# Kernel tuning notes

Measured on AMD Instinct MI355X. Metric: run time of the kernel, lower is better.

## Reference

```python
import jax, jax.numpy as jnp
import numpy as np

N_NODES = 50000
N_EDGES = 800000
IN_DIM = 128
HID_DIM = 128
N_GRAPHS = 512


def setup_inputs() -> dict:
    key = jax.random.key(0)
    ks = jax.random.split(key, 8)
    x = jax.random.normal(ks[0], (N_NODES, IN_DIM), dtype=jnp.float32)
    edge_index = jax.random.randint(ks[1], (2, N_EDGES), 0, N_NODES, dtype=jnp.int64)
    batch = jnp.sort(jax.random.randint(ks[2], (N_NODES,), 0, N_GRAPHS, dtype=jnp.int64))
    x_source = jax.random.randint(ks[3], (N_NODES,), 0, 2, dtype=jnp.int64)
    s1 = 1.0 / np.sqrt(IN_DIM)
    s2 = 1.0 / np.sqrt(HID_DIM)
    W1 = jax.random.normal(ks[4], (IN_DIM, HID_DIM), dtype=jnp.float32) * s1
    b1 = jnp.zeros((HID_DIM,), dtype=jnp.float32)
    W2 = jax.random.normal(ks[5], (HID_DIM, HID_DIM), dtype=jnp.float32) * s2
    b2 = jnp.zeros((HID_DIM,), dtype=jnp.float32)
    Wh = jax.random.normal(ks[6], (HID_DIM + IN_DIM, 2), dtype=jnp.float32) * (1.0 / np.sqrt(HID_DIM + IN_DIM))
    bh = jnp.zeros((2,), dtype=jnp.float32)
    return {"x": x, "edge_index": edge_index, "batch": batch, "x_source": x_source,
            "W1": W1, "b1": b1, "W2": W2, "b2": b2, "Wh": Wh, "bh": bh}


def _gcn_conv(x, W, b, src, dst, deg_inv_sqrt):
    # PyG GCNConv: h = x W; out[i] = sum_{j->i} norm_ij h[j] + norm_ii h[i] + b
    # with self-loops and symmetric normalization norm_ij = d_i^{-1/2} d_j^{-1/2}
    h = x @ W                                        # [N, out]
    norm_e = deg_inv_sqrt[src] * deg_inv_sqrt[dst]    # [E]
    msg = h[src] * norm_e[:, None]                    # gather + scale
    agg = jax.ops.segment_sum(msg, dst, num_segments=x.shape[0])
    agg = agg + h * (deg_inv_sqrt ** 2)[:, None]      # self-loop term
    return agg + b


def _mean_pool(x, seg, num_segments):
    sums = jax.ops.segment_sum(x, seg, num_segments=num_segments)
    cnt = jax.ops.segment_sum(jnp.ones((x.shape[0],), x.dtype), seg, num_segments=num_segments)
    return sums / jnp.maximum(cnt, 1.0)[:, None]


def reference(x, edge_index, batch, x_source, W1, b1, W2, b2, Wh, bh):
    src, dst = edge_index[0], edge_index[1]
    # degree with self-loops (edge weights = 1)
    deg = jax.ops.segment_sum(jnp.ones((src.shape[0],), x.dtype), dst,
                              num_segments=x.shape[0]) + 1.0
    deg_inv_sqrt = jax.lax.rsqrt(deg)

    h = jax.nn.relu(_gcn_conv(x, W1, b1, src, dst, deg_inv_sqrt))
    # dropout is identity in eval mode
    h = jax.nn.relu(_gcn_conv(h, W2, b2, src, dst, deg_inv_sqrt))

    gnn_emb = _mean_pool(h, batch, N_GRAPHS)          # [G, hid]

    # CodeBERT pooling: masked mean of raw node features where x_source == 1
    mask = (x_source == 1).astype(x.dtype)            # [N]
    summed = jax.ops.segment_sum(x * mask[:, None], batch, num_segments=N_GRAPHS)
    counts = jnp.maximum(jax.ops.segment_sum(mask, batch, num_segments=N_GRAPHS), 1.0)
    codebert_emb = summed / counts[:, None]           # [G, in]

    emb = jnp.concatenate([gnn_emb, codebert_emb], axis=1)  # [G, hid+in]
    return emb @ Wh + bh                              # [G, 2]
```

## Files before the change

### kernel.cpp

```cpp
#include <hip/hip_runtime.h>
#include <hip/hip_fp16.h>

#define NNODES 50000
#define NEDGES 800000
#define DIM    128
#define NGRAPH 512
#define NSLAB  3125
#define EPB    1024
#define NBLK_E 782
#define NBUCK  196
#define HSTRIDE NBLK_E
#define NHIST  (NBUCK * HSTRIDE)
#define NSB1   ((NHIST + 255) / 256)

typedef _Float16 f16x8 __attribute__((ext_vector_type(8)));
typedef float    f32x4 __attribute__((ext_vector_type(4)));
union U4H8 { uint4 u; f16x8 h; };

__global__ void prep_w(const float* __restrict__ W1, const float* __restrict__ W2,
                       __half* __restrict__ Wt1, __half* __restrict__ Wt2) {
    int i = blockIdx.x * 256 + threadIdx.x;
    if (i >= 4096) return;
    const float* W = (i < 2048) ? W1 : W2;
    __half* Wt = (i < 2048) ? Wt1 : Wt2;
    int j = i & 2047;
    int c  = j >> 4;
    int k0 = (j & 15) * 8;
    __half tmp[8];
    #pragma unroll
    for (int u = 0; u < 8; ++u) tmp[u] = (__half)W[(size_t)(k0 + u) * DIM + c];
    *(uint4*)(Wt + (size_t)c * DIM + k0) = *(uint4*)tmp;
}

__global__ void __launch_bounds__(256) bucket_hist(const int* __restrict__ dst,
                                                   int* __restrict__ hist) {
    __shared__ int cnt[NBUCK];
    int t = threadIdx.x;
    if (t < NBUCK) cnt[t] = 0;
    __syncthreads();
    int e0 = blockIdx.x * EPB + t * 4;
    if (e0 + 3 < NEDGES) {
        int4 d = *(const int4*)(dst + e0);
        atomicAdd(&cnt[d.x >> 8], 1);
        atomicAdd(&cnt[d.y >> 8], 1);
        atomicAdd(&cnt[d.z >> 8], 1);
        atomicAdd(&cnt[d.w >> 8], 1);
    }
    __syncthreads();
    if (t < NBUCK) hist[t * HSTRIDE + blockIdx.x] = cnt[t];
}

__global__ void sb1(const int* __restrict__ in, int* __restrict__ out,
                    int* __restrict__ partials) {
    __shared__ int s[256];
    int t = threadIdx.x;
    int gid = blockIdx.x * 256 + t;
    int v = (gid < NHIST) ? in[gid] : 0;
    s[t] = v;
    __syncthreads();
    #pragma unroll
    for (int o = 1; o < 256; o <<= 1) {
        int u = (t >= o) ? s[t - o] : 0;
        __syncthreads();
        s[t] += u;
        __syncthreads();
    }
    if (gid < NHIST) out[gid] = s[t] - v;
    if (t == 255) partials[blockIdx.x] = s[255];
}

__global__ void sb2(int* __restrict__ partials) {
    __shared__ int s[1024];
    int t = threadIdx.x;
    int v = (t < NSB1) ? partials[t] : 0;
    s[t] = v;
    __syncthreads();
    #pragma unroll
    for (int o = 1; o < 1024; o <<= 1) {
        int u = (t >= o) ? s[t - o] : 0;
        __syncthreads();
        s[t] += u;
        __syncthreads();
    }
    if (t < NSB1) partials[t] = s[t] - v;
}

__global__ void sb3(int* __restrict__ hist, const int* __restrict__ partials) {
    int gid = blockIdx.x * 256 + threadIdx.x;
    if (gid < NHIST) hist[gid] += partials[blockIdx.x];
}

__global__ void __launch_bounds__(256) bucket_scatter(const int* __restrict__ src,
                                                      const int* __restrict__ dst,
                                                      const int* __restrict__ hist,
                                                      int2* __restrict__ ebuf) {
    __shared__ int cnt[NBUCK];
    __shared__ int base[NBUCK];
    int t = threadIdx.x;
    if (t < NBUCK) { cnt[t] = 0; base[t] = hist[t * HSTRIDE + blockIdx.x]; }
    __syncthreads();
    int e0 = blockIdx.x * EPB + t * 4;
    if (e0 + 3 < NEDGES) {
        int4 s = *(const int4*)(src + e0);
        int4 d = *(const int4*)(dst + e0);
        int b, r;
        b = d.x >> 8; r = atomicAdd(&cnt[b], 1); ebuf[base[b] + r] = make_int2(s.x, d.x);
        b = d.y >> 8; r = atomicAdd(&cnt[b], 1); ebuf[base[b] + r] = make_int2(s.y, d.y);
        b = d.z >> 8; r = atomicAdd(&cnt[b], 1); ebuf[base[b] + r] = make_int2(s.z, d.z);
        b = d.w >> 8; r = atomicAdd(&cnt[b], 1); ebuf[base[b] + r] = make_int2(s.w, d.w);
    }
}

__global__ void __launch_bounds__(256) node_sort(const int2* __restrict__ ebuf,
                                                 const int* __restrict__ hist,
                                                 int* __restrict__ rowstart,
                                                 float* __restrict__ dis,
                                                 int* __restrict__ csr_src) {
    __shared__ int cnt[256], cnt2[256], off[256], s[256];
    int b = blockIdx.x;
    int t = threadIdx.x;
    int start = hist[b * HSTRIDE];
    int end = (b + 1 < NBUCK) ? hist[(b + 1) * HSTRIDE] : NEDGES;
    cnt[t] = 0; cnt2[t] = 0;
    __syncthreads();
    for (int i = start + t; i < end; i += 256)
        atomicAdd(&cnt[ebuf[i].y & 255], 1);
    __syncthreads();
    s[t] = cnt[t];
    __syncthreads();
    #pragma unroll
    for (int o = 1; o < 256; o <<= 1) {
        int u = (t >= o) ? s[t - o] : 0;
        __syncthreads();
        s[t] += u;
        __syncthreads();
    }
    off[t] = s[t] - cnt[t];
    int node = b * 256 + t;
    if (node < NNODES) {
        rowstart[node] = start + off[t];
        dis[node] = rsqrtf((float)cnt[t] + 1.0f);
    }
    if (b == NBUCK - 1 && t == 0) rowstart[NNODES] = NEDGES;
    __syncthreads();
    for (int i = start + t; i < end; i += 256) {
        int2 e = ebuf[i];
        int j = e.y & 255;
        int r = atomicAdd(&cnt2[j], 1);
        csr_src[start + off[j] + r] = e.x;
    }
}

template<typename XT>
__global__ void __launch_bounds__(256) gemm_mfma(const XT* __restrict__ X,
                                                 const __half* __restrict__ Wt,
                                                 const float* __restrict__ dis,
                                                 __half* __restrict__ Y) {
    __shared__ __align__(16) unsigned char Wl[128 * 256];

    const int t = threadIdx.x;
    {
        int col = t >> 1;
        int kb0 = (t & 1) * 128;
        const unsigned char* g = (const unsigned char*)Wt + col * 256 + kb0;
        #pragma unroll
        for (int i = 0; i < 8; ++i) {
            uint4 v = *(const uint4*)(g + i * 16);
            int kb = kb0 + i * 16;
            *(uint4*)(Wl + col * 256 + (kb ^ ((col & 7) << 4))) = v;
        }
    }
    __syncthreads();

    int wave = t >> 6;
    int slab = blockIdx.x * 4 + wave;
    if (slab >= NSLAB) return;
    int l  = t & 63;
    int lr = l & 15;
    int lg = l >> 4;

    int arow = slab * 16 + lr;

    f16x8 afr[4];
    if constexpr (sizeof(XT) == 4) {
        const float* xr = (const float*)X + (size_t)arow * DIM;
        #pragma unroll
        for (int c = 0; c < 4; ++c) {
            int k0 = c * 32 + lg * 8;
            float4 u0 = *(const float4*)(xr + k0);
            float4 u1 = *(const float4*)(xr + k0 + 4);
            f16x8 a;
            a[0] = (_Float16)u0.x; a[1] = (_Float16)u0.y;
            a[2] = (_Float16)u0.z; a[3] = (_Float16)u0.w;
            a[4] = (_Float16)u1.x; a[5] = (_Float16)u1.y;
            a[6] = (_Float16)u1.z; a[7] = (_Float16)u1.w;
            afr[c] = a;
        }
    } else {
        const __half* xr = (const __half*)X + (size_t)arow * DIM;
        #pragma unroll
        for (int c = 0; c < 4; ++c) {
            U4H8 u; u.u = *(const uint4*)(xr + c * 32 + lg * 8);
            afr[c] = u.h;
        }
    }

    f32x4 acc[8];
    #pragma unroll
    for (int jt = 0; jt < 8; ++jt) acc[jt] = (f32x4){0.f, 0.f, 0.f, 0.f};

    #pragma unroll
    for (int c = 0; c < 4; ++c) {
        #pragma unroll
        for (int jt = 0; jt < 8; ++jt) {
            int col = jt * 16 + lr;
            int kb  = c * 64 + lg * 16;
            U4H8 bb;
            bb.u = *(const uint4*)(Wl + col * 256 + (kb ^ ((col & 7) << 4)));
            acc[jt] = __builtin_amdgcn_mfma_f32_16x16x32_f16(afr[c], bb.h, acc[jt], 0, 0, 0);
        }
    }

    float4 dv = *(const float4*)(dis + slab * 16 + lg * 4);
    float dsc[4] = {dv.x, dv.y, dv.z, dv.w};
    #pragma unroll
    for (int j = 0; j < 4; ++j) {
        int row = slab * 16 + lg * 4 + j;
        __half* yr = Y + (size_t)row * DIM + lr;
        #pragma unroll
        for (int jt = 0; jt < 8; ++jt)
            yr[jt * 16] = (__half)(acc[jt][j] * dsc[j]);
    }
}

__device__ __forceinline__ void acc_add(float4& a, uint2 u) {
    float2 f0 = __half22float2(*(__half2*)&u.x);
    float2 f1 = __half22float2(*(__half2*)&u.y);
    a.x += f0.x; a.y += f0.y; a.z += f1.x; a.w += f1.y;
}

__global__ void __launch_bounds__(256) gcn_gather(const __half* __restrict__ hwh,
                                                  const int* __restrict__ rowstart,
                                                  const int* __restrict__ csr_src,
                                                  const float* __restrict__ dis,
                                                  const float* __restrict__ b,
                                                  __half* __restrict__ outh) {
    int t = blockIdx.x * 256 + threadIdx.x;
    int d = t >> 5, q = t & 31;
    if (d >= NNODES) return;
    const uint2* hw8 = (const uint2*)hwh;

    float4 a0 = make_float4(0.f, 0.f, 0.f, 0.f);
    float4 a1 = a0, a2 = a0, a3 = a0, a4 = a0, a5 = a0, a6 = a0, a7 = a0;

    acc_add(a0, hw8[(size_t)d * 32 + q]);

    int beg = rowstart[d], end = rowstart[d + 1];
    int i = beg;
    for (; i + 8 <= end; i += 8) {
        int s0 = csr_src[i + 0], s1 = csr_src[i + 1];
        int s2 = csr_src[i + 2], s3 = csr_src[i + 3];
        int s4 = csr_src[i + 4], s5 = csr_src[i + 5];
        int s6 = csr_src[i + 6], s7 = csr_src[i + 7];
        uint2 v0 = hw8[(size_t)s0 * 32 + q];
        uint2 v1 = hw8[(size_t)s1 * 32 + q];
        uint2 v2 = hw8[(size_t)s2 * 32 + q];
        uint2 v3 = hw8[(size_t)s3 * 32 + q];
        uint2 v4 = hw8[(size_t)s4 * 32 + q];
        uint2 v5 = hw8[(size_t)s5 * 32 + q];
        uint2 v6 = hw8[(size_t)s6 * 32 + q];
        uint2 v7 = hw8[(size_t)s7 * 32 + q];
        acc_add(a0, v0); acc_add(a1, v1); acc_add(a2, v2); acc_add(a3, v3);
        acc_add(a4, v4); acc_add(a5, v5); acc_add(a6, v6); acc_add(a7, v7);
    }
    for (; i + 2 <= end; i += 2) {
        uint2 v0 = hw8[(size_t)csr_src[i + 0] * 32 + q];
        uint2 v1 = hw8[(size_t)csr_src[i + 1] * 32 + q];
        acc_add(a0, v0); acc_add(a1, v1);
    }
    if (i < end) acc_add(a0, hw8[(size_t)csr_src[i] * 32 + q]);

    a0.x += a1.x + a2.x + a3.x + a4.x + a5.x + a6.x + a7.x;
    a0.y += a1.y + a2.y + a3.y + a4.y + a5.y + a6.y + a7.y;
    a0.z += a1.z + a2.z + a3.z + a4.z + a5.z + a6.z + a7.z;
    a0.w += a1.w + a2.w + a3.w + a4.w + a5.w + a6.w + a7.w;

    float dd = dis[d];
    float4 bb = ((const float4*)b)[q];
    __half ot[4];
    ot[0] = (__half)fmaxf(fmaf(a0.x, dd, bb.x), 0.f);
    ot[1] = (__half)fmaxf(fmaf(a0.y, dd, bb.y), 0.f);
    ot[2] = (__half)fmaxf(fmaf(a0.z, dd, bb.z), 0.f);
    ot[3] = (__half)fmaxf(fmaf(a0.w, dd, bb.w), 0.f);
    ((uint2*)outh)[(size_t)d * 32 + q] = *(uint2*)ot;
}

__device__ __forceinline__ int lower_bound_i(const int* __restrict__ a, int n, int v) {
    int lo = 0, hi = n;
    while (lo < hi) {
        int mid = (lo + hi) >> 1;
        if (a[mid] < v) lo = mid + 1; else hi = mid;
    }
    return lo;
}

__global__ void __launch_bounds__(256) pool_head(const __half* __restrict__ h,
                                                 const float* __restrict__ x,
                                                 const int* __restrict__ batch,
                                                 const int* __restrict__ xsrc,
                                                 const float* __restrict__ Wh,
                                                 const float* __restrict__ bh,
                                                 float* __restrict__ out) {
    __shared__ float sAG[DIM];
    __shared__ float sAC[DIM];
    __shared__ int   sSC;
    int g   = blockIdx.x;
    int t   = threadIdx.x;
    int sub = t >> 5;
    int q   = t & 31;

    if (t < DIM) { sAG[t] = 0.f; sAC[t] = 0.f; }
    if (t == 0) sSC = 0;
    __syncthreads();

    int lo = lower_bound_i(batch, NNODES, g);
    int hi = lower_bound_i(batch, NNODES, g + 1);

    float4 ag = make_float4(0.f, 0.f, 0.f, 0.f);
    float4 ac = make_float4(0.f, 0.f, 0.f, 0.f);
    int sc = 0;
    const uint2* h8 = (const uint2*)h;
    const float4* x4 = (const float4*)x;
    for (int r = lo + sub; r < hi; r += 8) {
        acc_add(ag, h8[(size_t)r * 32 + q]);
        if (xsrc[r] == 1) {
            float4 xv = x4[(size_t)r * 32 + q];
            ac.x += xv.x; ac.y += xv.y; ac.z += xv.z; ac.w += xv.w;
            sc++;
        }
    }
    float* agp = sAG + q * 4;
    atomicAdd(agp + 0, ag.x); atomicAdd(agp + 1, ag.y);
    atomicAdd(agp + 2, ag.z); atomicAdd(agp + 3, ag.w);
    float* acp = sAC + q * 4;
    atomicAdd(acp + 0, ac.x); atomicAdd(acp + 1, ac.y);
    atomicAdd(acp + 2, ac.z); atomicAdd(acp + 3, ac.w);
    if (q == 0 && sc) atomicAdd(&sSC, sc);
    __syncthreads();

    if (t < 32) {
        float invg = 1.0f / fmaxf((float)(hi - lo), 1.0f);
        float invc = 1.0f / fmaxf((float)sSC, 1.0f);
        const float2* Wh2 = (const float2*)Wh;
        float a0 = 0.f, a1 = 0.f;
        #pragma unroll
        for (int j = 0; j < 4; ++j) {
            float e1 = sAG[t * 4 + j] * invg;
            float2 w1 = Wh2[t * 4 + j];
            a0 = fmaf(e1, w1.x, a0);
            a1 = fmaf(e1, w1.y, a1);
            float e2 = sAC[t * 4 + j] * invc;
            float2 w2 = Wh2[DIM + t * 4 + j];
            a0 = fmaf(e2, w2.x, a0);
            a1 = fmaf(e2, w2.y, a1);
        }
        #pragma unroll
        for (int off = 16; off; off >>= 1) {
            a0 += __shfl_down(a0, off, 32);
            a1 += __shfl_down(a1, off, 32);
        }
        if (t == 0) {
            out[g * 2 + 0] = a0 + bh[0];
            out[g * 2 + 1] = a1 + bh[1];
        }
    }
}

extern "C" void kernel_launch(void* const* d_in, const int* in_sizes, int n_in,
                              void* d_out, int out_size, void* d_ws, size_t ws_size,
                              hipStream_t stream) {
    const float* x     = (const float*)d_in[0];
    const int*   ei    = (const int*)d_in[1];
    const int*   batch = (const int*)d_in[2];
    const int*   xsrc  = (const int*)d_in[3];
    const float* W1 = (const float*)d_in[4];
    const float* b1 = (const float*)d_in[5];
    const float* W2 = (const float*)d_in[6];
    const float* b2 = (const float*)d_in[7];
    const float* Wh = (const float*)d_in[8];
    const float* bh = (const float*)d_in[9];
    float* out = (float*)d_out;

    const int* src = ei;
    const int* dst = ei + NEDGES;

    float* ws = (float*)d_ws;
    size_t off = 0;
    float*  dis      = ws + off;            off += 50048;
    int*    rowstart = (int*)(ws + off);    off += 50048;
    int*    hist     = (int*)(ws + off);    off += ((NHIST + 255) & ~255);
    int*    partials = (int*)(ws + off);    off += 1024;
    int2*   ebuf     = (int2*)(ws + off);   off += 2 * 800000;
    int*    csr_src  = (int*)(ws + off);    off += 800000;
    __half* Wt1      = (__half*)(ws + off); off += 8192;
    __half* Wt2      = (__half*)(ws + off); off += 8192;
    __half* hwh      = (__half*)(ws + off); off += (size_t)NNODES * DIM / 2;
    __half* hbuf     = (__half*)(ws + off); off += (size_t)NNODES * DIM / 2;

    prep_w<<<16, 256, 0, stream>>>(W1, W2, Wt1, Wt2);
    bucket_hist<<<NBLK_E, 256, 0, stream>>>(dst, hist);
    sb1<<<NSB1, 256, 0, stream>>>(hist, hist, partials);
    sb2<<<1, 1024, 0, stream>>>(partials);
    sb3<<<NSB1, 256, 0, stream>>>(hist, partials);
    bucket_scatter<<<NBLK_E, 256, 0, stream>>>(src, dst, hist, ebuf);
    node_sort<<<NBUCK, 256, 0, stream>>>(ebuf, hist, rowstart, dis, csr_src);

    const int ngemm = (NSLAB + 3) / 4;

    gemm_mfma<float><<<ngemm, 256, 0, stream>>>(x, Wt1, dis, hwh);
    gcn_gather<<<(NNODES * 32) / 256, 256, 0, stream>>>(hwh, rowstart, csr_src, dis, b1, hbuf);

    gemm_mfma<__half><<<ngemm, 256, 0, stream>>>(hbuf, Wt2, dis, hwh);
    gcn_gather<<<(NNODES * 32) / 256, 256, 0, stream>>>(hwh, rowstart, csr_src, dis, b2, hbuf);

    pool_head<<<NGRAPH, 256, 0, stream>>>(hbuf, x, batch, xsrc, Wh, bh, out);
}
```

Measured before the change: 151.1 us.

## Pack edge buffer to 32 bits, restructure bucket scan, fuse weight prep

Edges in the bucket buffer are now packed into one 32-bit word (16-bit source plus the low 8 bits of the destination) instead of an int2, which halves the traffic of the scatter and node-sort passes. The three-kernel global scan becomes a per-bucket scan plus a small scan of bucket totals. Weight transposition is folded into extra blocks of the histogram kernel, and each block now handles 2048 edges. Together these cut launches and preprocessing traffic, but the packing only works while node ids fit in 16 bits.

Measured after the change: 157.1 us. 1.04x slower.

```diff
diff --git a/kernel.cpp b/kernel.cpp
--- a/kernel.cpp
+++ b/kernel.cpp
@@ -6,56 +6,77 @@
 #define DIM    128
 #define NGRAPH 512
 #define NSLAB  3125
-#define EPB    1024
-#define NBLK_E 782
+#define EPB    2048
+#define NBLK_E 391
 #define NBUCK  196
 #define HSTRIDE NBLK_E
-#define NHIST  (NBUCK * HSTRIDE)
-#define NSB1   ((NHIST + 255) / 256)
 
 typedef _Float16 f16x8 __attribute__((ext_vector_type(8)));
 typedef float    f32x4 __attribute__((ext_vector_type(4)));
 union U4H8 { uint4 u; f16x8 h; };
 
-__global__ void prep_w(const float* __restrict__ W1, const float* __restrict__ W2,
-                       __half* __restrict__ Wt1, __half* __restrict__ Wt2) {
-    int i = blockIdx.x * 256 + threadIdx.x;
-    if (i >= 4096) return;
-    const float* W = (i < 2048) ? W1 : W2;
-    __half* Wt = (i < 2048) ? Wt1 : Wt2;
-    int j = i & 2047;
-    int c  = j >> 4;
-    int k0 = (j & 15) * 8;
-    __half tmp[8];
-    #pragma unroll
-    for (int u = 0; u < 8; ++u) tmp[u] = (__half)W[(size_t)(k0 + u) * DIM + c];
-    *(uint4*)(Wt + (size_t)c * DIM + k0) = *(uint4*)tmp;
-}
-
 __global__ void __launch_bounds__(256) bucket_hist(const int* __restrict__ dst,
-                                                   int* __restrict__ hist) {
+                                                   int* __restrict__ hist,
+                                                   const float* __restrict__ W1,
+                                                   const float* __restrict__ W2,
+                                                   __half* __restrict__ Wt1,
+                                                   __half* __restrict__ Wt2) {
+    int t = threadIdx.x;
+    if (blockIdx.x >= NBLK_E) {
+        int i = (blockIdx.x - NBLK_E) * 256 + t;
+        const float* W = (i < 2048) ? W1 : W2;
+        __half* Wt = (i < 2048) ? Wt1 : Wt2;
+        int j = i & 2047;
+        int c  = j >> 4;
+        int k0 = (j & 15) * 8;
+        __half tmp[8];
+        #pragma unroll
+        for (int u = 0; u < 8; ++u) tmp[u] = (__half)W[(size_t)(k0 + u) * DIM + c];
+        *(uint4*)(Wt + (size_t)c * DIM + k0) = *(uint4*)tmp;
+        return;
+    }
     __shared__ int cnt[NBUCK];
+    if (t < NBUCK) cnt[t] = 0;
+    __syncthreads();
+    int e0 = blockIdx.x * EPB + t * 8;
+    if (e0 + 7 < NEDGES) {
+        int4 d0 = *(const int4*)(dst + e0);
+        int4 d1 = *(const int4*)(dst + e0 + 4);
+        atomicAdd(&cnt[d0.x >> 8], 1);
+        atomicAdd(&cnt[d0.y >> 8], 1);
+        atomicAdd(&cnt[d0.z >> 8], 1);
+        atomicAdd(&cnt[d0.w >> 8], 1);
+        atomicAdd(&cnt[d1.x >> 8], 1);
+        atomicAdd(&cnt[d1.y >> 8], 1);
+        atomicAdd(&cnt[d1.z >> 8], 1);
+        atomicAdd(&cnt[d1.w >> 8], 1);
+    }
+    __syncthreads();
+    if (t < NBUCK) hist[t * HSTRIDE + blockIdx.x] = cnt[t];
+}
+
+__global__ void __launch_bounds__(512) scan1(int* __restrict__ hist, int* __restrict__ btot) {
+    __shared__ int s[512];
+    int b = blockIdx.x;
     int t = threadIdx.x;
-    if (t < NBUCK) cnt[t] = 0;
-    __syncthreads();
-    int e0 = blockIdx.x * EPB + t * 4;
-    if (e0 + 3 < NEDGES) {
-        int4 d = *(const int4*)(dst + e0);
-        atomicAdd(&cnt[d.x >> 8], 1);
-        atomicAdd(&cnt[d.y >> 8], 1);
-        atomicAdd(&cnt[d.z >> 8], 1);
-        atomicAdd(&cnt[d.w >> 8], 1);
-    }
-    __syncthreads();
-    if (t < NBUCK) hist[t * HSTRIDE + blockIdx.x] = cnt[t];
-}
-
-__global__ void sb1(const int* __restrict__ in, int* __restrict__ out,
-                    int* __restrict__ partials) {
+    int v = (t < HSTRIDE) ? hist[b * HSTRIDE + t] : 0;
+    s[t] = v;
+    __syncthreads();
+    #pragma unroll
+    for (int o = 1; o < 512; o <<= 1) {
+        int u = (t >= o) ? s[t - o] : 0;
+        __syncthreads();
+        s[t] += u;
+        __syncthreads();
+    }
+    if (t < HSTRIDE) hist[b * HSTRIDE + t] = s[t] - v;
+    if (t == 511) btot[b] = s[511];
+}
+
+__global__ void __launch_bounds__(256) scan2(const int* __restrict__ btot, int* __restrict__ base) {
     __shared__ int s[256];
     int t = threadIdx.x;
-    int gid = blockIdx.x * 256 + t;
-    int v = (gid < NHIST) ? in[gid] : 0;
+    int v = (t < NBUCK) ? btot[t] : 0;
     s[t] = v;
     __syncthreads();
     #pragma unroll
@@ -65,66 +86,52 @@
         s[t] += u;
         __syncthreads();
     }
-    if (gid < NHIST) out[gid] = s[t] - v;
-    if (t == 255) partials[blockIdx.x] = s[255];
-}
-
-__global__ void sb2(int* __restrict__ partials) {
-    __shared__ int s[1024];
-    int t = threadIdx.x;
-    int v = (t < NSB1) ? partials[t] : 0;
-    s[t] = v;
-    __syncthreads();
-    #pragma unroll
-    for (int o = 1; o < 1024; o <<= 1) {
-        int u = (t >= o) ? s[t - o] : 0;
-        __syncthreads();
-        s[t] += u;
-        __syncthreads();
-    }
-    if (t < NSB1) partials[t] = s[t] - v;
-}
-
-__global__ void sb3(int* __restrict__ hist, const int* __restrict__ partials) {
-    int gid = blockIdx.x * 256 + threadIdx.x;
-    if (gid < NHIST) hist[gid] += partials[blockIdx.x];
+    if (t < NBUCK) base[t] = s[t] - v;
+    if (t == 255) base[NBUCK] = s[255];
 }
 
 __global__ void __launch_bounds__(256) bucket_scatter(const int* __restrict__ src,
                                                       const int* __restrict__ dst,
                                                       const int* __restrict__ hist,
-                                                      int2* __restrict__ ebuf) {
+                                                      const int* __restrict__ base,
+                                                      unsigned* __restrict__ ebuf) {
     __shared__ int cnt[NBUCK];
-    __shared__ int base[NBUCK];
+    __shared__ int sbase[NBUCK];
     int t = threadIdx.x;
-    if (t < NBUCK) { cnt[t] = 0; base[t] = hist[t * HSTRIDE + blockIdx.x]; }
-    __syncthreads();
-    int e0 = blockIdx.x * EPB + t * 4;
-    if (e0 + 3 < NEDGES) {
-        int4 s = *(const int4*)(src + e0);
-        int4 d = *(const int4*)(dst + e0);
+    if (t < NBUCK) { cnt[t] = 0; sbase[t] = base[t] + hist[t * HSTRIDE + blockIdx.x]; }
+    __syncthreads();
+    int e0 = blockIdx.x * EPB + t * 8;
+    if (e0 + 7 < NEDGES) {
+        int4 s0 = *(const int4*)(src + e0);
+        int4 s1 = *(const int4*)(src + e0 + 4);
+        int4 d0 = *(const int4*)(dst + e0);
+        int4 d1 = *(const int4*)(dst + e0 + 4);
         int b, r;
-        b = d.x >> 8; r = atomicAdd(&cnt[b], 1); ebuf[base[b] + r] = make_int2(s.x, d.x);
-        b = d.y >> 8; r = atomicAdd(&cnt[b], 1); ebuf[base[b] + r] = make_int2(s.y, d.y);
-        b = d.z >> 8; r = atomicAdd(&cnt[b], 1); ebuf[base[b] + r] = make_int2(s.z, d.z);
-        b = d.w >> 8; r = atomicAdd(&cnt[b], 1); ebuf[base[b] + r] = make_int2(s.w, d.w);
-    }
-}
-
-__global__ void __launch_bounds__(256) node_sort(const int2* __restrict__ ebuf,
-                                                 const int* __restrict__ hist,
+        b = d0.x >> 8; r = atomicAdd(&cnt[b], 1); ebuf[sbase[b] + r] = (unsigned)s0.x | ((unsigned)(d0.x & 255) << 16);
+        b = d0.y >> 8; r = atomicAdd(&cnt[b], 1); ebuf[sbase[b] + r] = (unsigned)s0.y | ((unsigned)(d0.y & 255) << 16);
+        b = d0.z >> 8; r = atomicAdd(&cnt[b], 1); ebuf[sbase[b] + r] = (unsigned)s0.z | ((unsigned)(d0.z & 255) << 16);
+        b = d0.w >> 8; r = atomicAdd(&cnt[b], 1); ebuf[sbase[b] + r] = (unsigned)s0.w | ((unsigned)(d0.w & 255) << 16);
+        b = d1.x >> 8; r = atomicAdd(&cnt[b], 1); ebuf[sbase[b] + r] = (unsigned)s1.x | ((unsigned)(d1.x & 255) << 16);
+        b = d1.y >> 8; r = atomicAdd(&cnt[b], 1); ebuf[sbase[b] + r] = (unsigned)s1.y | ((unsigned)(d1.y & 255) << 16);
+        b = d1.z >> 8; r = atomicAdd(&cnt[b], 1); ebuf[sbase[b] + r] = (unsigned)s1.z | ((unsigned)(d1.z & 255) << 16);
+        b = d1.w >> 8; r = atomicAdd(&cnt[b], 1); ebuf[sbase[b] + r] = (unsigned)s1.w | ((unsigned)(d1.w & 255) << 16);
+    }
+}
+
+__global__ void __launch_bounds__(256) node_sort(const unsigned* __restrict__ ebuf,
+                                                 const int* __restrict__ base,
                                                  int* __restrict__ rowstart,
                                                  float* __restrict__ dis,
                                                  int* __restrict__ csr_src) {
     __shared__ int cnt[256], cnt2[256], off[256], s[256];
     int b = blockIdx.x;
     int t = threadIdx.x;
-    int start = hist[b * HSTRIDE];
-    int end = (b + 1 < NBUCK) ? hist[(b + 1) * HSTRIDE] : NEDGES;
+    int start = base[b];
+    int end   = base[b + 1];
     cnt[t] = 0; cnt2[t] = 0;
     __syncthreads();
     for (int i = start + t; i < end; i += 256)
-        atomicAdd(&cnt[ebuf[i].y & 255], 1);
+        atomicAdd(&cnt[(ebuf[i] >> 16) & 255], 1);
     __syncthreads();
     s[t] = cnt[t];
     __syncthreads();
@@ -144,10 +151,10 @@
     if (b == NBUCK - 1 && t == 0) rowstart[NNODES] = NEDGES;
     __syncthreads();
     for (int i = start + t; i < end; i += 256) {
-        int2 e = ebuf[i];
-        int j = e.y & 255;
+        unsigned e = ebuf[i];
+        int j = (e >> 16) & 255;
         int r = atomicAdd(&cnt2[j], 1);
-        csr_src[start + off[j] + r] = e.x;
+        csr_src[start + off[j] + r] = (int)(e & 0xFFFFu);
     }
 }
 
@@ -396,24 +403,23 @@
 
     float* ws = (float*)d_ws;
     size_t off = 0;
-    float*  dis      = ws + off;            off += 50048;
-    int*    rowstart = (int*)(ws + off);    off += 50048;
-    int*    hist     = (int*)(ws + off);    off += ((NHIST + 255) & ~255);
-    int*    partials = (int*)(ws + off);    off += 1024;
-    int2*   ebuf     = (int2*)(ws + off);   off += 2 * 800000;
-    int*    csr_src  = (int*)(ws + off);    off += 800000;
-    __half* Wt1      = (__half*)(ws + off); off += 8192;
-    __half* Wt2      = (__half*)(ws + off); off += 8192;
-    __half* hwh      = (__half*)(ws + off); off += (size_t)NNODES * DIM / 2;
-    __half* hbuf     = (__half*)(ws + off); off += (size_t)NNODES * DIM / 2;
-
-    prep_w<<<16, 256, 0, stream>>>(W1, W2, Wt1, Wt2);
-    bucket_hist<<<NBLK_E, 256, 0, stream>>>(dst, hist);
-    sb1<<<NSB1, 256, 0, stream>>>(hist, hist, partials);
-    sb2<<<1, 1024, 0, stream>>>(partials);
-    sb3<<<NSB1, 256, 0, stream>>>(hist, partials);
-    bucket_scatter<<<NBLK_E, 256, 0, stream>>>(src, dst, hist, ebuf);
-    node_sort<<<NBUCK, 256, 0, stream>>>(ebuf, hist, rowstart, dis, csr_src);
+    float*    dis      = ws + off;              off += 50048;
+    int*      rowstart = (int*)(ws + off);      off += 50048;
+    int*      hist     = (int*)(ws + off);      off += NBUCK * HSTRIDE + 64;
+    int*      btot     = (int*)(ws + off);      off += 256;
+    int*      base     = (int*)(ws + off);      off += 256;
+    unsigned* ebuf     = (unsigned*)(ws + off); off += 800000;
+    int*      csr_src  = (int*)(ws + off);      off += 800000;
+    __half*   Wt1      = (__half*)(ws + off);   off += 8192;
+    __half*   Wt2      = (__half*)(ws + off);   off += 8192;
+    __half*   hwh      = (__half*)(ws + off);   off += (size_t)NNODES * DIM / 2;
+    __half*   hbuf     = (__half*)(ws + off);   off += (size_t)NNODES * DIM / 2;
+
+    bucket_hist<<<NBLK_E + 16, 256, 0, stream>>>(dst, hist, W1, W2, Wt1, Wt2);
+    scan1<<<NBUCK, 512, 0, stream>>>(hist, btot);
+    scan2<<<1, 256, 0, stream>>>(btot, base);
+    bucket_scatter<<<NBLK_E, 256, 0, stream>>>(src, dst, hist, base, ebuf);
+    node_sort<<<NBUCK, 256, 0, stream>>>(ebuf, base, rowstart, dis, csr_src);
 
     const int ngemm = (NSLAB + 3) / 4;
 
```
